# Optimization experiments

Measured on AMD Instinct MI355X. Metric: run time of the kernel, lower is better.

The kernel has to match this reference:

```python
import jax, jax.numpy as jnp
import numpy as np

KLEN = 3  # kernel_len, since input_F has 9 = 3**2 channels


def local_crf(F, Q):
    """Per-pixel dynamic local filtering.
    F: [b, K*K, h, w] per-pixel kernel weights
    Q: [b, g, h, w] features
    out[b,g,i,j] = sum_k F[b,k,i,j] * Q[b,g,i+di_k,j+dj_k] (zero-padded 'same').
    """
    b, g, h, w = Q.shape
    p = KLEN // 2
    Qp = jnp.pad(Q, ((0, 0), (0, 0), (p, p), (p, p)))
    out = jnp.zeros_like(Q)
    k = 0
    for di in range(KLEN):
        for dj in range(KLEN):
            out = out + F[:, k][:, None] * Qp[:, :, di:di + h, dj:dj + w]
            k += 1
    return out


def setup_inputs() -> dict:
    key = jax.random.key(0)
    k1, k2, k3 = jax.random.split(key, 3)
    b, C, G, h, w = 4, 19, 8, 512, 512
    input_F = jax.random.uniform(k1, (b, KLEN * KLEN, h, w), dtype=jnp.float32)
    input_logit = jax.random.normal(k2, (b, C, h, w), dtype=jnp.float32)
    matrix = jax.random.uniform(k3, (G, C, 1, 1), dtype=jnp.float32, minval=-0.05, maxval=0.05)
    return {"input_F": input_F, "input_logit": input_logit, "matrix": matrix}


def reference(input_F, input_logit, matrix):
    # softmax over categories
    Q = jax.nn.softmax(input_logit, axis=1)                 # [b,C,h,w]
    # encoding matrix: softmax over groups of sharpened params; 1x1 conv == einsum
    E = jax.nn.softmax(100.0 * matrix, axis=0)[:, :, 0, 0]  # [G,C]
    Qg = jnp.einsum('gc,bchw->bghw', E, Q)                  # encode C -> G
    out = local_crf(input_F, Qg)                            # [b,G,h,w]
    out = jnp.einsum('gc,bghw->bchw', E, out)               # decode G -> C (E^T)
    return input_logit - out
```

## Files before the change

### kernel.cpp

```cpp
#include <hip/hip_runtime.h>

#define C_DIM 19
#define G_DIM 8
#define H_DIM 512
#define W_DIM 512
#define B_DIM 4
#define PLANE (H_DIM * W_DIM)
#define NPIX  (B_DIM * PLANE)
#define NT    256
#define TLX   64
#define TLY   8
#define HXX   (TLX + 2)
#define HYY   (TLY + 2)

__device__ __forceinline__ unsigned bf16rne(float f) {
    unsigned x = __float_as_uint(f);
    return (x + 0x7fffu + ((x >> 16) & 1u)) >> 16;
}
__device__ __forceinline__ float up_lo(unsigned u) { return __uint_as_float(u << 16); }
__device__ __forceinline__ float up_hi(unsigned u) { return __uint_as_float(u & 0xffff0000u); }

__device__ __forceinline__ float2 ntload2(const float* p) {
    unsigned long long v = __builtin_nontemporal_load((const unsigned long long*)p);
    float2 r;
    r.x = __uint_as_float((unsigned)v);
    r.y = __uint_as_float((unsigned)(v >> 32));
    return r;
}
__device__ __forceinline__ void ntstore2(float* p, float f0, float f1) {
    unsigned long long v = (unsigned long long)__float_as_uint(f0) |
                           ((unsigned long long)__float_as_uint(f1) << 32);
    __builtin_nontemporal_store(v, (unsigned long long*)p);
}

__device__ __forceinline__ void build_E_nosync(const float* __restrict__ matrix,
                                               float4 (*E4)[2], int tid) {
    if (tid < C_DIM) {
        const int c = tid;
        float m[G_DIM];
        float mx = -1e30f;
        #pragma unroll
        for (int g = 0; g < G_DIM; ++g) {
            m[g] = 100.0f * matrix[g * C_DIM + c];
            mx = fmaxf(mx, m[g]);
        }
        float s = 0.0f;
        #pragma unroll
        for (int g = 0; g < G_DIM; ++g) { m[g] = __expf(m[g] - mx); s += m[g]; }
        const float inv = 1.0f / s;
        E4[c][0] = make_float4(m[0]*inv, m[1]*inv, m[2]*inv, m[3]*inv);
        E4[c][1] = make_float4(m[4]*inv, m[5]*inv, m[6]*inv, m[7]*inv);
    }
}

__global__ __launch_bounds__(NT, 4)
void qg_encode(const float* __restrict__ logit,
               const float* __restrict__ matrix,
               uint4* __restrict__ Qg)
{
    __shared__ float4 E4[C_DIM][2];
    build_E_nosync(matrix, E4, threadIdx.x);
    __syncthreads();

    const int bid = blockIdx.x;
    const int swz = (bid & 7) * (NPIX / (2 * NT) / 8) + (bid >> 3);
    const int t   = swz * NT + threadIdx.x;
    const int px0 = t * 2;
    const int b   = px0 >> 18;
    const int pix = px0 & (PLANE - 1);
    const float* __restrict__ p = logit + (size_t)b * C_DIM * PLANE + pix;

    float eg[G_DIM][2];
    #pragma unroll
    for (int g = 0; g < G_DIM; ++g) { eg[g][0] = 0.0f; eg[g][1] = 0.0f; }
    float s0 = 0.0f, s1 = 0.0f;

    #pragma unroll
    for (int c = 0; c < C_DIM; ++c) {
        const float2 lv = *(const float2*)(p + (size_t)c * PLANE);
        const float e0 = __expf(lv.x);
        const float e1 = __expf(lv.y);
        s0 += e0; s1 += e1;
        const float4 E0 = E4[c][0];
        const float4 E1 = E4[c][1];
        eg[0][0] = fmaf(E0.x, e0, eg[0][0]);  eg[0][1] = fmaf(E0.x, e1, eg[0][1]);
        eg[1][0] = fmaf(E0.y, e0, eg[1][0]);  eg[1][1] = fmaf(E0.y, e1, eg[1][1]);
        eg[2][0] = fmaf(E0.z, e0, eg[2][0]);  eg[2][1] = fmaf(E0.z, e1, eg[2][1]);
        eg[3][0] = fmaf(E0.w, e0, eg[3][0]);  eg[3][1] = fmaf(E0.w, e1, eg[3][1]);
        eg[4][0] = fmaf(E1.x, e0, eg[4][0]);  eg[4][1] = fmaf(E1.x, e1, eg[4][1]);
        eg[5][0] = fmaf(E1.y, e0, eg[5][0]);  eg[5][1] = fmaf(E1.y, e1, eg[5][1]);
        eg[6][0] = fmaf(E1.z, e0, eg[6][0]);  eg[6][1] = fmaf(E1.z, e1, eg[6][1]);
        eg[7][0] = fmaf(E1.w, e0, eg[7][0]);  eg[7][1] = fmaf(E1.w, e1, eg[7][1]);
    }
    {
        const float inv = 1.0f / s0;
        uint4 u;
        u.x = bf16rne(eg[0][0]*inv) | (bf16rne(eg[1][0]*inv) << 16);
        u.y = bf16rne(eg[2][0]*inv) | (bf16rne(eg[3][0]*inv) << 16);
        u.z = bf16rne(eg[4][0]*inv) | (bf16rne(eg[5][0]*inv) << 16);
        u.w = bf16rne(eg[6][0]*inv) | (bf16rne(eg[7][0]*inv) << 16);
        Qg[px0] = u;
    }
    {
        const float inv = 1.0f / s1;
        uint4 u;
        u.x = bf16rne(eg[0][1]*inv) | (bf16rne(eg[1][1]*inv) << 16);
        u.y = bf16rne(eg[2][1]*inv) | (bf16rne(eg[3][1]*inv) << 16);
        u.z = bf16rne(eg[4][1]*inv) | (bf16rne(eg[5][1]*inv) << 16);
        u.w = bf16rne(eg[6][1]*inv) | (bf16rne(eg[7][1]*inv) << 16);
        Qg[px0 + 1] = u;
    }
}

__global__ __launch_bounds__(NT, 4)
void crf_decode(const float* __restrict__ F,
                const float* __restrict__ logit,
                const float* __restrict__ matrix,
                const uint4* __restrict__ Qg,
                float* __restrict__ out)
{
    __shared__ float4 E4[C_DIM][2];
    __shared__ uint4  Qs[HYY][HXX];

    const int tid = threadIdx.x;
    build_E_nosync(matrix, E4, tid);

    const int bid = (blockIdx.z * gridDim.y + blockIdx.y) * gridDim.x + blockIdx.x;
    const int swz = (bid & 7) * 256 + (bid >> 3);
    const int b   = swz >> 9;
    const int rem = swz & 511;
    const int tby = rem >> 3;
    const int tbx = rem & 7;

    const int tx2 = tid & 31;
    const int ty  = tid >> 5;
    const int x   = tbx * TLX + tx2 * 2;
    const int y   = tby * TLY + ty;
    const size_t pix = (size_t)y * W_DIM + x;

    const float* __restrict__ Fp = F + (size_t)b * 9 * PLANE + pix;
    float2 wk[9];
    #pragma unroll
    for (int k = 0; k < 9; ++k) wk[k] = ntload2(Fp + (size_t)k * PLANE);

    const int y0 = tby * TLY - 1;
    const int x0 = tbx * TLX - 1;
    const uint4* __restrict__ Qb = Qg + (size_t)b * PLANE;
    #pragma unroll
    for (int it = 0; it < 3; ++it) {
        const int i = tid + it * NT;
        if (i < HYY * HXX) {
            const int r  = i / HXX;
            const int cc = i - r * HXX;
            const int gy = min(max(y0 + r, 0), H_DIM - 1);
            const int gx = min(max(x0 + cc, 0), W_DIM - 1);
            Qs[r][cc] = Qb[(size_t)gy * W_DIM + gx];
        }
    }
    __syncthreads();

    const float* __restrict__ lp = logit + (size_t)b * C_DIM * PLANE + pix;
    float2 l0 = *(const float2*)(lp + 0 * (size_t)PLANE);
    float2 l1 = *(const float2*)(lp + 1 * (size_t)PLANE);
    float2 l2 = *(const float2*)(lp + 2 * (size_t)PLANE);
    float2 l3 = *(const float2*)(lp + 3 * (size_t)PLANE);
    float2 l4 = *(const float2*)(lp + 4 * (size_t)PLANE);
    float2 l5 = *(const float2*)(lp + 5 * (size_t)PLANE);
    float2 l6 = *(const float2*)(lp + 6 * (size_t)PLANE);
    float2 l7 = *(const float2*)(lp + 7 * (size_t)PLANE);

    float og[G_DIM][2];
    #pragma unroll
    for (int g = 0; g < G_DIM; ++g) { og[g][0] = 0.0f; og[g][1] = 0.0f; }

    const int lx = tx2 * 2;
    #pragma unroll
    for (int dyi = 0; dyi < 3; ++dyi) {
        const int ry  = y + dyi - 1;
        const bool vy = (ry >= 0) & (ry < H_DIM);
        const uint4 q0 = Qs[ty + dyi][lx];
        const uint4 q1 = Qs[ty + dyi][lx + 1];
        const uint4 q2 = Qs[ty + dyi][lx + 2];
        const uint4 q3 = Qs[ty + dyi][lx + 3];
        const uint4 qv_[4] = {q0, q1, q2, q3};

        #pragma unroll
        for (int dxi = 0; dxi < 3; ++dxi) {
            const int k = dyi * 3 + dxi;
            const float wkv[2] = {wk[k].x, wk[k].y};
            #pragma unroll
            for (int j = 0; j < 2; ++j) {
                const int col = x + j + dxi - 1;
                const bool v = vy & (col >= 0) & (col < W_DIM);
                const float wv = v ? wkv[j] : 0.0f;
                const uint4 qv = qv_[j + dxi];
                og[0][j] = fmaf(wv, up_lo(qv.x), og[0][j]);
                og[1][j] = fmaf(wv, up_hi(qv.x), og[1][j]);
                og[2][j] = fmaf(wv, up_lo(qv.y), og[2][j]);
                og[3][j] = fmaf(wv, up_hi(qv.y), og[3][j]);
                og[4][j] = fmaf(wv, up_lo(qv.z), og[4][j]);
                og[5][j] = fmaf(wv, up_hi(qv.z), og[5][j]);
                og[6][j] = fmaf(wv, up_lo(qv.w), og[6][j]);
                og[7][j] = fmaf(wv, up_hi(qv.w), og[7][j]);
            }
        }
    }

    float* __restrict__ op = out + (size_t)b * C_DIM * PLANE + pix;
    #pragma unroll
    for (int c = 0; c < C_DIM; ++c) {
        const float2 cur = l0;
        l0 = l1; l1 = l2; l2 = l3; l3 = l4; l4 = l5; l5 = l6; l6 = l7;
        if (c + 8 < C_DIM)
            l7 = *(const float2*)(lp + (size_t)(c + 8) * PLANE);

        const float4 E0 = E4[c][0];
        const float4 E1 = E4[c][1];
        float d0 = og[0][0] * E0.x;
        float d1 = og[0][1] * E0.x;
        d0 = fmaf(og[1][0], E0.y, d0);  d1 = fmaf(og[1][1], E0.y, d1);
        d0 = fmaf(og[2][0], E0.z, d0);  d1 = fmaf(og[2][1], E0.z, d1);
        d0 = fmaf(og[3][0], E0.w, d0);  d1 = fmaf(og[3][1], E0.w, d1);
        d0 = fmaf(og[4][0], E1.x, d0);  d1 = fmaf(og[4][1], E1.x, d1);
        d0 = fmaf(og[5][0], E1.y, d0);  d1 = fmaf(og[5][1], E1.y, d1);
        d0 = fmaf(og[6][0], E1.z, d0);  d1 = fmaf(og[6][1], E1.z, d1);
        d0 = fmaf(og[7][0], E1.w, d0);  d1 = fmaf(og[7][1], E1.w, d1);

        ntstore2(op + (size_t)c * PLANE, cur.x - d0, cur.y - d1);
    }
}

extern "C" void kernel_launch(void* const* d_in, const int* in_sizes, int n_in,
                              void* d_out, int out_size, void* d_ws, size_t ws_size,
                              hipStream_t stream) {
    const float* F      = (const float*)d_in[0];
    const float* logit  = (const float*)d_in[1];
    const float* matrix = (const float*)d_in[2];
    float* out = (float*)d_out;
    uint4* Qg = (uint4*)d_ws;

    qg_encode <<<NPIX / (2 * NT), NT, 0, stream>>>(logit, matrix, Qg);
    dim3 grid2(W_DIM / TLX, H_DIM / TLY, B_DIM);
    crf_decode<<<grid2, NT, 0, stream>>>(F, logit, matrix, Qg, out);
}
```

Before: 52.46 us.

## Split local filter and channel decode into separate kernels via fp32 workspace

After: 70.00 us. 33.4% more time.

```diff
diff --git a/kernel.cpp b/kernel.cpp
--- a/kernel.cpp
+++ b/kernel.cpp
@@ -113,17 +113,13 @@
 }
 
 __global__ __launch_bounds__(NT, 4)
-void crf_decode(const float* __restrict__ F,
-                const float* __restrict__ logit,
-                const float* __restrict__ matrix,
+void crf_filter(const float* __restrict__ F,
                 const uint4* __restrict__ Qg,
-                float* __restrict__ out)
+                float* __restrict__ og_ws)
 {
-    __shared__ float4 E4[C_DIM][2];
-    __shared__ uint4  Qs[HYY][HXX];
+    __shared__ uint4 Qs[HYY][HXX];
 
     const int tid = threadIdx.x;
-    build_E_nosync(matrix, E4, tid);
 
     const int bid = (blockIdx.z * gridDim.y + blockIdx.y) * gridDim.x + blockIdx.x;
     const int swz = (bid & 7) * 256 + (bid >> 3);
@@ -158,16 +154,6 @@
         }
     }
     __syncthreads();
-
-    const float* __restrict__ lp = logit + (size_t)b * C_DIM * PLANE + pix;
-    float2 l0 = *(const float2*)(lp + 0 * (size_t)PLANE);
-    float2 l1 = *(const float2*)(lp + 1 * (size_t)PLANE);
-    float2 l2 = *(const float2*)(lp + 2 * (size_t)PLANE);
-    float2 l3 = *(const float2*)(lp + 3 * (size_t)PLANE);
-    float2 l4 = *(const float2*)(lp + 4 * (size_t)PLANE);
-    float2 l5 = *(const float2*)(lp + 5 * (size_t)PLANE);
-    float2 l6 = *(const float2*)(lp + 6 * (size_t)PLANE);
-    float2 l7 = *(const float2*)(lp + 7 * (size_t)PLANE);
 
     float og[G_DIM][2];
     #pragma unroll
@@ -206,27 +192,54 @@
         }
     }
 
+    float4* __restrict__ op = (float4*)(og_ws + ((size_t)b * PLANE + pix) * G_DIM);
+    op[0] = make_float4(og[0][0], og[1][0], og[2][0], og[3][0]);
+    op[1] = make_float4(og[4][0], og[5][0], og[6][0], og[7][0]);
+    op[2] = make_float4(og[0][1], og[1][1], og[2][1], og[3][1]);
+    op[3] = make_float4(og[4][1], og[5][1], og[6][1], og[7][1]);
+}
+
+__global__ __launch_bounds__(NT, 4)
+void crf_decode2(const float* __restrict__ logit,
+                 const float* __restrict__ matrix,
+                 const float* __restrict__ og_ws,
+                 float* __restrict__ out)
+{
+    __shared__ float4 E4[C_DIM][2];
+    build_E_nosync(matrix, E4, threadIdx.x);
+    __syncthreads();
+
+    const int bid = blockIdx.x;
+    const int swz = (bid & 7) * (NPIX / (2 * NT) / 8) + (bid >> 3);
+    const int t   = swz * NT + threadIdx.x;
+    const int px0 = t * 2;
+    const int b   = px0 >> 18;
+    const int pix = px0 & (PLANE - 1);
+
+    const float4* __restrict__ ogp = (const float4*)(og_ws + (size_t)px0 * G_DIM);
+    const float4 A0 = ogp[0];
+    const float4 B0 = ogp[1];
+    const float4 A1 = ogp[2];
+    const float4 B1 = ogp[3];
+
+    const float* __restrict__ lp = logit + (size_t)b * C_DIM * PLANE + pix;
     float* __restrict__ op = out + (size_t)b * C_DIM * PLANE + pix;
+
     #pragma unroll
     for (int c = 0; c < C_DIM; ++c) {
-        const float2 cur = l0;
-        l0 = l1; l1 = l2; l2 = l3; l3 = l4; l4 = l5; l5 = l6; l6 = l7;
-        if (c + 8 < C_DIM)
-            l7 = *(const float2*)(lp + (size_t)(c + 8) * PLANE);
-
+        const float2 lv = *(const float2*)(lp + (size_t)c * PLANE);
         const float4 E0 = E4[c][0];
         const float4 E1 = E4[c][1];
-        float d0 = og[0][0] * E0.x;
-        float d1 = og[0][1] * E0.x;
-        d0 = fmaf(og[1][0], E0.y, d0);  d1 = fmaf(og[1][1], E0.y, d1);
-        d0 = fmaf(og[2][0], E0.z, d0);  d1 = fmaf(og[2][1], E0.z, d1);
-        d0 = fmaf(og[3][0], E0.w, d0);  d1 = fmaf(og[3][1], E0.w, d1);
-        d0 = fmaf(og[4][0], E1.x, d0);  d1 = fmaf(og[4][1], E1.x, d1);
-        d0 = fmaf(og[5][0], E1.y, d0);  d1 = fmaf(og[5][1], E1.y, d1);
-        d0 = fmaf(og[6][0], E1.z, d0);  d1 = fmaf(og[6][1], E1.z, d1);
-        d0 = fmaf(og[7][0], E1.w, d0);  d1 = fmaf(og[7][1], E1.w, d1);
-
-        ntstore2(op + (size_t)c * PLANE, cur.x - d0, cur.y - d1);
+        float d0 = A0.x * E0.x;
+        float d1 = A1.x * E0.x;
+        d0 = fmaf(A0.y, E0.y, d0);  d1 = fmaf(A1.y, E0.y, d1);
+        d0 = fmaf(A0.z, E0.z, d0);  d1 = fmaf(A1.z, E0.z, d1);
+        d0 = fmaf(A0.w, E0.w, d0);  d1 = fmaf(A1.w, E0.w, d1);
+        d0 = fmaf(B0.x, E1.x, d0);  d1 = fmaf(B1.x, E1.x, d1);
+        d0 = fmaf(B0.y, E1.y, d0);  d1 = fmaf(B1.y, E1.y, d1);
+        d0 = fmaf(B0.z, E1.z, d0);  d1 = fmaf(B1.z, E1.z, d1);
+        d0 = fmaf(B0.w, E1.w, d0);  d1 = fmaf(B1.w, E1.w, d1);
+        ntstore2(op + (size_t)c * PLANE, lv.x - d0, lv.y - d1);
     }
 }
 
@@ -237,9 +250,12 @@
     const float* logit  = (const float*)d_in[1];
     const float* matrix = (const float*)d_in[2];
     float* out = (float*)d_out;
-    uint4* Qg = (uint4*)d_ws;
-
-    qg_encode <<<NPIX / (2 * NT), NT, 0, stream>>>(logit, matrix, Qg);
+
+    uint4* Qg    = (uint4*)d_ws;
+    float* og_ws = (float*)((char*)d_ws + (size_t)NPIX * 16);
+
+    qg_encode  <<<NPIX / (2 * NT), NT, 0, stream>>>(logit, matrix, Qg);
     dim3 grid2(W_DIM / TLX, H_DIM / TLY, B_DIM);
-    crf_decode<<<grid2, NT, 0, stream>>>(F, logit, matrix, Qg, out);
-}
+    crf_filter <<<grid2, NT, 0, stream>>>(F, Qg, og_ws);
+    crf_decode2<<<NPIX / (2 * NT), NT, 0, stream>>>(logit, matrix, og_ws, out);
+}
```
